# Kernel optimization log

Hardware: AMD Instinct MI355X
Metric: run time of the kernel (lower is better)

Reference implementation:

```python
import jax, jax.numpy as jnp
import numpy as np

NUM_FORMULAS = 256
NUM_CONJ_ARR = [6, 9, 12, 15]
DEPTH_ARR = [2, 4, 6]
TEMPERATURE = 2.0
INPUT_DIM = 512
BATCH = 8192

# --- static DNF structure (mirrors build-time indicator matrices) ---
_group = NUM_FORMULAS // len(NUM_CONJ_ARR)                       # 64 formulas per group
_conj_per_formula = np.repeat(np.array(NUM_CONJ_ARR), _group)     # [F]
_CONJ2FORM = np.repeat(np.arange(NUM_FORMULAS), _conj_per_formula)  # [C] = 2688
TOTAL_CONJ = int(_CONJ2FORM.shape[0])
_depths = np.tile(np.array(DEPTH_ARR), TOTAL_CONJ // len(DEPTH_ARR))  # depth per conjunction
_LIT2CONJ = np.repeat(np.arange(TOTAL_CONJ), _depths)             # [L] = 10752
TOTAL_LIT = int(_LIT2CONJ.shape[0])


def setup_inputs() -> dict:
    key = jax.random.key(0)
    k = jax.random.split(key, 6)
    x = jax.random.normal(k[0], (BATCH, INPUT_DIM), jnp.float32)
    # literals_random_mask: binary feature-subset mask per literal (build-time constant)
    random_mask = (jax.random.uniform(k[1], (INPUT_DIM, TOTAL_LIT)) < 0.5).astype(jnp.float32)
    glorot = jnp.sqrt(2.0 / (INPUT_DIM + TOTAL_LIT))
    # weight is pre-multiplied by the random mask at build time
    weight = jax.random.normal(k[2], (INPUT_DIM, TOTAL_LIT), jnp.float32) * glorot * random_mask
    # learnable_binary_mask: soft binary-threshold output in [0, 1]
    learnable_binary_mask = jax.random.uniform(k[3], (INPUT_DIM, TOTAL_LIT), jnp.float32)
    bias = jnp.zeros((TOTAL_LIT,), jnp.float32)
    mu = jax.random.normal(k[4], (NUM_FORMULAS, INPUT_DIM), jnp.float32)
    sigma = 1.0 + 0.1 * jax.random.uniform(k[5], (NUM_FORMULAS,), jnp.float32)
    return {
        "x": x, "weight": weight, "learnable_binary_mask": learnable_binary_mask,
        "bias": bias, "mu": mu, "sigma": sigma,
        "lit2conj": jnp.asarray(_LIT2CONJ, jnp.int32),
        "conj2form": jnp.asarray(_CONJ2FORM, jnp.int32),
    }


def reference(x, weight, learnable_binary_mask, bias, mu, sigma, lit2conj, conj2form):
    # literal projection: tanh(x @ (W * M) + b)             -> [B, L]
    literals = jnp.tanh(x @ (weight * learnable_binary_mask) + bias)
    # soft AND over literals of each conjunction: tanh(sum - d + 1.5)
    and_bias = jax.ops.segment_sum(jnp.ones((TOTAL_LIT,), literals.dtype), lit2conj,
                                   num_segments=TOTAL_CONJ)
    conj_sum = jax.ops.segment_sum(literals.T, lit2conj, num_segments=TOTAL_CONJ).T  # [B, C]
    conj = jnp.tanh(conj_sum - and_bias + 1.5)
    # soft OR over conjunctions of each formula: tanh(sum + d - 1.5)
    or_bias = jax.ops.segment_sum(jnp.ones((TOTAL_CONJ,), conj.dtype), conj2form,
                                  num_segments=NUM_FORMULAS)
    form_sum = jax.ops.segment_sum(conj.T, conj2form, num_segments=NUM_FORMULAS).T   # [B, F]
    dnnf = jnp.tanh(form_sum + or_bias - 1.5)
    # localization: softmax over formulas of temperature-scaled RBF, via GEMM expansion
    sq = (jnp.sum(x * x, axis=1, keepdims=True) - 2.0 * (x @ mu.T)
          + jnp.sum(mu * mu, axis=1)[None, :])                                       # [B, F]
    loc = jax.nn.softmax(TEMPERATURE * jnp.exp(-0.5 * sq / (sigma * sigma)[None, :]), axis=-1)
    return dnnf * loc
```

## Files before the change

### kernel.cpp

```cpp
#include <hip/hip_runtime.h>


#define BATCH 8192
#define IDIM 512
#define NFORM 256
#define NLIT 10752
#define WT_ROWS 11136

#define BM 128
#define BN 192
#define BK 64
#define BUFB 40960
#define SLITP 196

typedef __bf16 bf16x8 __attribute__((ext_vector_type(8)));
typedef float f32x4 __attribute__((ext_vector_type(4)));
typedef unsigned short u16;
typedef unsigned int u32;

__device__ __forceinline__ u16 f2bf(float f) {
  u32 u = __float_as_uint(f);
  u = (u + 0x7fffu + ((u >> 16) & 1u)) >> 16;
  return (u16)u;
}

__device__ __forceinline__ float fast_tanh(float x) {
  float e = __expf(2.0f * x);
  return 1.0f - 2.0f * __builtin_amdgcn_rcpf(e + 1.0f);
}

__device__ __forceinline__ void async_cp16(const void* g, void* l) {
  __builtin_amdgcn_global_load_lds(
      (const u32 __attribute__((address_space(1)))*)g,
      (u32 __attribute__((address_space(3)))*)l, 16, 0, 0);
}


#define PREPX_BLKS 2048
#define PREPW_BLKS 1344

__global__ __launch_bounds__(256) void prep_all(
    const float* __restrict__ x, const float* __restrict__ W,
    const float* __restrict__ M, const float* __restrict__ mu,
    u16* __restrict__ xb, u16* __restrict__ wt, float* __restrict__ xsq,
    float* __restrict__ musq, float* __restrict__ form_sum) {
  __shared__ float lds[64 * 65];
  const int blk = blockIdx.x, tid = threadIdx.x;

  if (blk < PREPX_BLKS) {
    ((uint4*)form_sum)[blk * 256 + tid] = make_uint4(0, 0, 0, 0);
    int wave = tid >> 6, lane = tid & 63;
    int row = blk * 4 + wave;
    const float4* px = (const float4*)(x + (size_t)row * IDIM);
    float4 a = px[lane * 2], b = px[lane * 2 + 1];
    uint4 pk;
    pk.x = (u32)f2bf(a.x) | ((u32)f2bf(a.y) << 16);
    pk.y = (u32)f2bf(a.z) | ((u32)f2bf(a.w) << 16);
    pk.z = (u32)f2bf(b.x) | ((u32)f2bf(b.y) << 16);
    pk.w = (u32)f2bf(b.z) | ((u32)f2bf(b.w) << 16);
    ((uint4*)(xb + (size_t)row * IDIM))[lane] = pk;
    float s = a.x * a.x + a.y * a.y + a.z * a.z + a.w * a.w +
              b.x * b.x + b.y * b.y + b.z * b.z + b.w * b.w;
#pragma unroll
    for (int o = 32; o > 0; o >>= 1) s += __shfl_down(s, o);
    if (lane == 0) xsq[row] = s;
  } else if (blk < PREPX_BLKS + PREPW_BLKS) {
    int b = blk - PREPX_BLKS;
    int l0 = (b % 168) * 64, k0 = (b / 168) * 64;
#pragma unroll
    for (int j = 0; j < 4; ++j) {
      int idx = tid + j * 256;
      int kk = idx >> 4, l4 = idx & 15;
      size_t g = (size_t)(k0 + kk) * NLIT + l0 + l4 * 4;
      float4 w4 = *(const float4*)(W + g);
      float4 m4 = *(const float4*)(M + g);
      lds[kk * 65 + l4 * 4 + 0] = w4.x * m4.x;
      lds[kk * 65 + l4 * 4 + 1] = w4.y * m4.y;
      lds[kk * 65 + l4 * 4 + 2] = w4.z * m4.z;
      lds[kk * 65 + l4 * 4 + 3] = w4.w * m4.w;
    }
    __syncthreads();
    int l = tid >> 2, kq = tid & 3;
    u32 pk[8];
#pragma unroll
    for (int t = 0; t < 8; ++t) {
      u16 lo = f2bf(lds[(kq * 16 + 2 * t) * 65 + l]);
      u16 hi = f2bf(lds[(kq * 16 + 2 * t + 1) * 65 + l]);
      pk[t] = (u32)lo | ((u32)hi << 16);
    }
    u32* dst = (u32*)(wt + (size_t)(l0 + l) * IDIM + k0 + kq * 16);
    ((uint4*)dst)[0] = make_uint4(pk[0], pk[1], pk[2], pk[3]);
    ((uint4*)dst)[1] = make_uint4(pk[4], pk[5], pk[6], pk[7]);
  } else {
    int b = blk - PREPX_BLKS - PREPW_BLKS;
    if (b < 256) {
      float s = 0.f;
#pragma unroll
      for (int j = tid; j < IDIM; j += 256) {
        float v = mu[(size_t)b * IDIM + j];
        wt[(size_t)(NLIT + b) * IDIM + j] = f2bf(v);
        s += v * v;
      }
      float* red = lds;
      red[tid] = s;
      __syncthreads();
      for (int sh = 128; sh > 0; sh >>= 1) {
        if (tid < sh) red[tid] += red[tid + sh];
        __syncthreads();
      }
      if (tid == 0) musq[b] = red[0];
    } else {
      int row = NLIT + 256 + (b - 256);
      for (int j = tid; j < IDIM; j += 256) wt[(size_t)row * IDIM + j] = 0;
    }
  }
}


__global__ __launch_bounds__(256, 2) void dnnf_gemm(
    const u16* __restrict__ xb, const u16* __restrict__ wt,
    const float* __restrict__ bias, float* __restrict__ form_sum,
    float* __restrict__ dotbuf) {
  __shared__ __align__(16) char smraw[2 * BUFB];
  float* slit = (float*)smraw;

  const int tid = threadIdx.x;
  const int wave = tid >> 6, lane = tid & 63;
  const int wm = wave & 1, wn = wave >> 1;
  const int m0 = blockIdx.x * BM, n0 = blockIdx.y * BN;
  const int q = lane >> 4, cn = lane & 15;

  const int kg8 = ((tid & 7) ^ ((tid >> 3) & 7)) * 8;
  const u16* pa = xb + (size_t)(m0 + (tid >> 3)) * IDIM + kg8;
  const u16* pb = wt + (size_t)(n0 + (tid >> 3)) * IDIM + kg8;
  const int dA = tid * 16;
  const int dB = 16384 + tid * 16;

  const int kg0_16 = ((q ^ (cn & 7)) << 4);
  int offA[4], offB[6];
#pragma unroll
  for (int mf = 0; mf < 4; ++mf)
    offA[mf] = (wm * 64 + mf * 16 + cn) * 128 + kg0_16;
#pragma unroll
  for (int nf = 0; nf < 6; ++nf)
    offB[nf] = 16384 + (wn * 96 + nf * 16 + cn) * 128 + kg0_16;

  f32x4 acc[4][6];
#pragma unroll
  for (int a = 0; a < 4; ++a)
#pragma unroll
    for (int b = 0; b < 6; ++b) acc[a][b] = (f32x4){0.f, 0.f, 0.f, 0.f};

#pragma unroll
  for (int i = 0; i < 4; ++i)
    async_cp16(pa + (size_t)i * 32 * IDIM, smraw + dA + i * 4096);
#pragma unroll
  for (int i = 0; i < 6; ++i)
    async_cp16(pb + (size_t)i * 32 * IDIM, smraw + dB + i * 4096);
  pa += BK;
  pb += BK;

#pragma unroll
  for (int kt = 0; kt < 8; ++kt) {
    const char* bufc = smraw + (kt & 1) * BUFB;
    if (kt < 7) {
      char* bufn = smraw + ((kt + 1) & 1) * BUFB;
#pragma unroll
      for (int i = 0; i < 4; ++i)
        async_cp16(pa + (size_t)i * 32 * IDIM, bufn + dA + i * 4096);
#pragma unroll
      for (int i = 0; i < 6; ++i)
        async_cp16(pb + (size_t)i * 32 * IDIM, bufn + dB + i * 4096);
      pa += BK;
      pb += BK;
      asm volatile("s_waitcnt vmcnt(10)\n\ts_barrier" ::: "memory");
    } else {
      asm volatile("s_waitcnt vmcnt(0)\n\ts_barrier" ::: "memory");
    }
#pragma unroll
    for (int ks = 0; ks < 2; ++ks) {
      const int x64 = ks ? 64 : 0;
      bf16x8 af[4], bfr[6];
#pragma unroll
      for (int mf = 0; mf < 4; ++mf)
        af[mf] = *(const bf16x8*)(bufc + (offA[mf] ^ x64));
#pragma unroll
      for (int nf = 0; nf < 6; ++nf)
        bfr[nf] = *(const bf16x8*)(bufc + (offB[nf] ^ x64));
#pragma unroll
      for (int mf = 0; mf < 4; ++mf)
#pragma unroll
        for (int nf = 0; nf < 6; ++nf)
          acc[mf][nf] = __builtin_amdgcn_mfma_f32_16x16x32_bf16(
              af[mf], bfr[nf], acc[mf][nf], 0, 0, 0);
    }
    if (kt < 7)
      asm volatile("s_waitcnt lgkmcnt(0)\n\ts_barrier" ::: "memory");
  }
  __syncthreads();

  if (n0 < NLIT) {
    float bv[6];
#pragma unroll
    for (int nf = 0; nf < 6; ++nf) bv[nf] = bias[n0 + wn * 96 + nf * 16 + cn];

#pragma unroll
    for (int ph = 0; ph < 2; ++ph) {
      if (ph) __syncthreads();
      if (wm == ph) {
#pragma unroll
        for (int nf = 0; nf < 6; ++nf) {
          int col = wn * 96 + nf * 16 + cn;
#pragma unroll
          for (int mf = 0; mf < 4; ++mf)
#pragma unroll
            for (int reg = 0; reg < 4; ++reg) {
              int lr = mf * 16 + q * 4 + reg;
              slit[lr * SLITP + col] = fast_tanh(acc[mf][nf][reg] + bv[nf]);
            }
        }
      }
      __syncthreads();

      int r = tid >> 2, sub = tid & 3;
      const float* lrow = slit + r * SLITP + sub * 48;
      int c0 = ((n0 + sub * 48) / 12) * 3;
      size_t grow = (size_t)(m0 + ph * 64 + r) * NFORM;
      float run = 0.f;
      int fprev = -1;
#pragma unroll
      for (int tr = 0; tr < 4; ++tr) {
        const float* p = lrow + tr * 12;
        float s2 = p[0] + p[1];
        float s4 = p[2] + p[3] + p[4] + p[5];
        float s6 = p[6] + p[7] + p[8] + p[9] + p[10] + p[11];
        float v = fast_tanh(s2 - 0.5f) + fast_tanh(s4 - 2.5f) +
                  fast_tanh(s6 - 4.5f);
        int c = c0 + tr * 3;
        int f = (c < 384)    ? (c / 6)
                : (c < 960)  ? 64 + (c - 384) / 9
                : (c < 1728) ? 128 + (c - 960) / 12
                             : 192 + (c - 1728) / 15;
        if (f != fprev) {
          if (fprev >= 0) atomicAdd(form_sum + grow + fprev, run);
          fprev = f;
          run = 0.f;
        }
        run += v;
      }
      atomicAdd(form_sum + grow + fprev, run);
    }
  } else {
#pragma unroll
    for (int nf = 0; nf < 6; ++nf) {
      int col = n0 - NLIT + wn * 96 + nf * 16 + cn;
      if (col < NFORM) {
#pragma unroll
        for (int mf = 0; mf < 4; ++mf)
#pragma unroll
          for (int reg = 0; reg < 4; ++reg) {
            int row = wm * 64 + mf * 16 + q * 4 + reg;
            dotbuf[(size_t)(m0 + row) * NFORM + col] = acc[mf][nf][reg];
          }
      }
    }
  }
}


__global__ __launch_bounds__(256) void finale(
    const float* __restrict__ form_sum, const float* __restrict__ dotbuf,
    const float* __restrict__ xsq, const float* __restrict__ musq,
    const float* __restrict__ sigma, float* __restrict__ out) {
  int wave = threadIdx.x >> 6, lane = threadIdx.x & 63;
  int r = blockIdx.x * 4 + wave;
  size_t base = (size_t)r * NFORM;
  float xs = xsq[r];
  float e[4], s = 0.f;
#pragma unroll
  for (int j = 0; j < 4; ++j) {
    int f = j * 64 + lane;
    float sq = xs - 2.0f * dotbuf[base + f] + musq[f];
    float sg = sigma[f];
    float p = __expf(-0.5f * sq / (sg * sg));
    e[j] = __expf(2.0f * p);
    s += e[j];
  }
#pragma unroll
  for (int o = 32; o > 0; o >>= 1) s += __shfl_xor(s, o);
  float inv = __builtin_amdgcn_rcpf(s);
#pragma unroll
  for (int j = 0; j < 4; ++j) {
    int f = j * 64 + lane;
    float dn = fast_tanh(form_sum[base + f] + (float)(6 + 3 * j) - 1.5f);
    out[base + f] = dn * e[j] * inv;
  }
}


extern "C" void kernel_launch(void* const* d_in, const int* in_sizes, int n_in,
                              void* d_out, int out_size, void* d_ws,
                              size_t ws_size, hipStream_t stream) {
  const float* x = (const float*)d_in[0];
  const float* W = (const float*)d_in[1];
  const float* M = (const float*)d_in[2];
  const float* bias = (const float*)d_in[3];
  const float* mu = (const float*)d_in[4];
  const float* sigma = (const float*)d_in[5];
  float* out = (float*)d_out;

  float* form_sum = (float*)d_ws;
  float* dotbuf = form_sum + (size_t)BATCH * NFORM;
  u16* xb = (u16*)(dotbuf + (size_t)BATCH * NFORM);
  u16* wt = xb + (size_t)BATCH * IDIM;
  float* xsq = (float*)(wt + (size_t)WT_ROWS * IDIM);
  float* musq = xsq + BATCH;

  prep_all<<<PREPX_BLKS + PREPW_BLKS + 384, 256, 0, stream>>>(
      x, W, M, mu, xb, wt, xsq, musq, form_sum);
  dnnf_gemm<<<dim3(BATCH / BM, WT_ROWS / BN), 256, 0, stream>>>(xb, wt, bias,
                                                                form_sum, dotbuf);
  finale<<<BATCH / 4, 256, 0, stream>>>(form_sum, dotbuf, xsq, musq, sigma, out);
}
```

Before: 239.0 us.

## Halve K-tile and shrink LDS footprint to fit three blocks per CU

Reduces the GEMM K-tile from 64 to 32, which halves the double-buffered LDS staging and re-derives the XOR swizzle for 64-byte rows. Launch bounds go from 2 to 3 blocks per CU to raise occupancy. The epilogue now processes 32-row chunks in four phases so the smaller LDS still holds the tanh scratch, and it reads literals with float4 loads. In exchange there are twice as many barriers and k-iterations, and register pressure under the tighter launch bound may cause spills.

```diff
diff --git a/kernel.cpp b/kernel.cpp
--- a/kernel.cpp
+++ b/kernel.cpp
@@ -9,8 +9,9 @@
 
 #define BM 128
 #define BN 192
-#define BK 64
-#define BUFB 40960
+#define BK 32
+#define ABYTES 8192
+#define BUFB 20480
 #define SLITP 196
 
 typedef __bf16 bf16x8 __attribute__((ext_vector_type(8)));
@@ -117,7 +118,7 @@
 }
 
 
-__global__ __launch_bounds__(256, 2) void dnnf_gemm(
+__global__ __launch_bounds__(256, 3) void dnnf_gemm(
     const u16* __restrict__ xb, const u16* __restrict__ wt,
     const float* __restrict__ bias, float* __restrict__ form_sum,
     float* __restrict__ dotbuf) {
@@ -130,20 +131,20 @@
   const int m0 = blockIdx.x * BM, n0 = blockIdx.y * BN;
   const int q = lane >> 4, cn = lane & 15;
 
-  const int kg8 = ((tid & 7) ^ ((tid >> 3) & 7)) * 8;
-  const u16* pa = xb + (size_t)(m0 + (tid >> 3)) * IDIM + kg8;
-  const u16* pb = wt + (size_t)(n0 + (tid >> 3)) * IDIM + kg8;
+  const int kgs = ((tid & 3) ^ ((tid >> 2) & 3) ^ ((tid >> 4) & 3)) * 8;
+  const u16* pa = xb + (size_t)(m0 + (tid >> 2)) * IDIM + kgs;
+  const u16* pb = wt + (size_t)(n0 + (tid >> 2)) * IDIM + kgs;
   const int dA = tid * 16;
-  const int dB = 16384 + tid * 16;
-
-  const int kg0_16 = ((q ^ (cn & 7)) << 4);
+  const int dB = ABYTES + tid * 16;
+
+  const int swz16 = (q ^ (cn & 3) ^ ((cn >> 2) & 3)) << 4;
   int offA[4], offB[6];
 #pragma unroll
   for (int mf = 0; mf < 4; ++mf)
-    offA[mf] = (wm * 64 + mf * 16 + cn) * 128 + kg0_16;
+    offA[mf] = (wm * 64 + mf * 16 + cn) * 64 + swz16;
 #pragma unroll
   for (int nf = 0; nf < 6; ++nf)
-    offB[nf] = 16384 + (wn * 96 + nf * 16 + cn) * 128 + kg0_16;
+    offB[nf] = ABYTES + (wn * 96 + nf * 16 + cn) * 64 + swz16;
 
   f32x4 acc[4][6];
 #pragma unroll
@@ -152,49 +153,45 @@
     for (int b = 0; b < 6; ++b) acc[a][b] = (f32x4){0.f, 0.f, 0.f, 0.f};
 
 #pragma unroll
-  for (int i = 0; i < 4; ++i)
-    async_cp16(pa + (size_t)i * 32 * IDIM, smraw + dA + i * 4096);
-#pragma unroll
-  for (int i = 0; i < 6; ++i)
-    async_cp16(pb + (size_t)i * 32 * IDIM, smraw + dB + i * 4096);
+  for (int i = 0; i < 2; ++i)
+    async_cp16(pa + (size_t)i * 64 * IDIM, smraw + dA + i * 4096);
+#pragma unroll
+  for (int i = 0; i < 3; ++i)
+    async_cp16(pb + (size_t)i * 64 * IDIM, smraw + dB + i * 4096);
   pa += BK;
   pb += BK;
 
 #pragma unroll
-  for (int kt = 0; kt < 8; ++kt) {
+  for (int kt = 0; kt < 16; ++kt) {
     const char* bufc = smraw + (kt & 1) * BUFB;
-    if (kt < 7) {
+    if (kt < 15) {
       char* bufn = smraw + ((kt + 1) & 1) * BUFB;
 #pragma unroll
-      for (int i = 0; i < 4; ++i)
-        async_cp16(pa + (size_t)i * 32 * IDIM, bufn + dA + i * 4096);
-#pragma unroll
-      for (int i = 0; i < 6; ++i)
-        async_cp16(pb + (size_t)i * 32 * IDIM, bufn + dB + i * 4096);
+      for (int i = 0; i < 2; ++i)
+        async_cp16(pa + (size_t)i * 64 * IDIM, bufn + dA + i * 4096);
+#pragma unroll
+      for (int i = 0; i < 3; ++i)
+        async_cp16(pb + (size_t)i * 64 * IDIM, bufn + dB + i * 4096);
       pa += BK;
       pb += BK;
-      asm volatile("s_waitcnt vmcnt(10)\n\ts_barrier" ::: "memory");
+      asm volatile("s_waitcnt vmcnt(5)\n\ts_barrier" ::: "memory");
     } else {
       asm volatile("s_waitcnt vmcnt(0)\n\ts_barrier" ::: "memory");
     }
-#pragma unroll
-    for (int ks = 0; ks < 2; ++ks) {
-      const int x64 = ks ? 64 : 0;
-      bf16x8 af[4], bfr[6];
-#pragma unroll
-      for (int mf = 0; mf < 4; ++mf)
-        af[mf] = *(const bf16x8*)(bufc + (offA[mf] ^ x64));
+    bf16x8 af[4], bfr[6];
+#pragma unroll
+    for (int mf = 0; mf < 4; ++mf)
+      af[mf] = *(const bf16x8*)(bufc + offA[mf]);
+#pragma unroll
+    for (int nf = 0; nf < 6; ++nf)
+      bfr[nf] = *(const bf16x8*)(bufc + offB[nf]);
+#pragma unroll
+    for (int mf = 0; mf < 4; ++mf)
 #pragma unroll
       for (int nf = 0; nf < 6; ++nf)
-        bfr[nf] = *(const bf16x8*)(bufc + (offB[nf] ^ x64));
-#pragma unroll
-      for (int mf = 0; mf < 4; ++mf)
-#pragma unroll
-        for (int nf = 0; nf < 6; ++nf)
-          acc[mf][nf] = __builtin_amdgcn_mfma_f32_16x16x32_bf16(
-              af[mf], bfr[nf], acc[mf][nf], 0, 0, 0);
-    }
-    if (kt < 7)
+        acc[mf][nf] = __builtin_amdgcn_mfma_f32_16x16x32_bf16(
+            af[mf], bfr[nf], acc[mf][nf], 0, 0, 0);
+    if (kt < 15)
       asm volatile("s_waitcnt lgkmcnt(0)\n\ts_barrier" ::: "memory");
   }
   __syncthreads();
@@ -205,35 +202,39 @@
     for (int nf = 0; nf < 6; ++nf) bv[nf] = bias[n0 + wn * 96 + nf * 16 + cn];
 
 #pragma unroll
-    for (int ph = 0; ph < 2; ++ph) {
+    for (int ph = 0; ph < 4; ++ph) {
       if (ph) __syncthreads();
-      if (wm == ph) {
-#pragma unroll
-        for (int nf = 0; nf < 6; ++nf) {
-          int col = wn * 96 + nf * 16 + cn;
-#pragma unroll
-          for (int mf = 0; mf < 4; ++mf)
+      if (wm == (ph >> 1)) {
+#pragma unroll
+        for (int mh = 0; mh < 2; ++mh) {
+          int mf = 2 * (ph & 1) + mh;
+#pragma unroll
+          for (int nf = 0; nf < 6; ++nf) {
+            int col = wn * 96 + nf * 16 + cn;
 #pragma unroll
             for (int reg = 0; reg < 4; ++reg) {
-              int lr = mf * 16 + q * 4 + reg;
-              slit[lr * SLITP + col] = fast_tanh(acc[mf][nf][reg] + bv[nf]);
+              int sr = mh * 16 + q * 4 + reg;
+              slit[sr * SLITP + col] = fast_tanh(acc[mf][nf][reg] + bv[nf]);
             }
+          }
         }
       }
       __syncthreads();
 
-      int r = tid >> 2, sub = tid & 3;
-      const float* lrow = slit + r * SLITP + sub * 48;
-      int c0 = ((n0 + sub * 48) / 12) * 3;
-      size_t grow = (size_t)(m0 + ph * 64 + r) * NFORM;
+      int r = tid >> 3, sub = tid & 7;
+      const float* lrow = slit + r * SLITP + sub * 24;
+      int c0 = ((n0 + sub * 24) / 12) * 3;
+      size_t grow = (size_t)(m0 + ph * 32 + r) * NFORM;
       float run = 0.f;
       int fprev = -1;
 #pragma unroll
-      for (int tr = 0; tr < 4; ++tr) {
-        const float* p = lrow + tr * 12;
-        float s2 = p[0] + p[1];
-        float s4 = p[2] + p[3] + p[4] + p[5];
-        float s6 = p[6] + p[7] + p[8] + p[9] + p[10] + p[11];
+      for (int tr = 0; tr < 2; ++tr) {
+        const float4 a0 = *(const float4*)(lrow + tr * 12);
+        const float4 a1 = *(const float4*)(lrow + tr * 12 + 4);
+        const float4 a2 = *(const float4*)(lrow + tr * 12 + 8);
+        float s2 = a0.x + a0.y;
+        float s4 = a0.z + a0.w + a1.x + a1.y;
+        float s6 = a1.z + a1.w + a2.x + a2.y + a2.z + a2.w;
         float v = fast_tanh(s2 - 0.5f) + fast_tanh(s4 - 2.5f) +
                   fast_tanh(s6 - 4.5f);
         int c = c0 + tr * 3;
```

Result: no change. 237.5 us (-0.7%).
